# Optimization experiments

Measured on AMD Instinct MI355X. Metric: run time of the kernel, lower is better.

The kernel has to match this reference:

```python
import jax, jax.numpy as jnp
import numpy as np

T, B = 21, 4096
H, E, V = 1024, 50, 96
PAD = 0


def setup_inputs() -> dict:
    key = jax.random.key(0)
    ks = jax.random.split(key, 10)
    s_e = 1.0 / np.sqrt(H)  # torch LSTM init scale
    emb = jax.random.normal(ks[0], (V, E), jnp.float32)
    emb = emb.at[PAD].set(0.0)  # padding_idx row is zero
    return {
        "input_ids": jax.random.randint(ks[1], (T, B), 0, V),
        "h0": jax.random.normal(ks[2], (1, B, H), jnp.float32),
        "c0": jax.random.normal(ks[3], (1, B, H), jnp.float32),
        "emb": emb,
        "W_ih": jax.random.uniform(ks[4], (4 * H, E), jnp.float32, -s_e, s_e),
        "W_hh": jax.random.uniform(ks[5], (4 * H, H), jnp.float32, -s_e, s_e),
        "b_ih": jax.random.uniform(ks[6], (4 * H,), jnp.float32, -s_e, s_e),
        "b_hh": jax.random.uniform(ks[7], (4 * H,), jnp.float32, -s_e, s_e),
        "W_out": jax.random.uniform(ks[8], (V, H), jnp.float32, -s_e, s_e),
        "b_out": jax.random.uniform(ks[9], (V,), jnp.float32, -s_e, s_e),
    }


def reference(input_ids, h0, c0, emb, W_ih, W_hh, b_ih, b_hh, W_out, b_out):
    # char_embeds: (T, B, E)
    x = emb[input_ids]
    # Precompute input projections for all timesteps in one GEMM: (T, B, 4H)
    x_proj = jnp.einsum("tbe,ge->tbg", x, W_ih) + b_ih + b_hh

    def step(carry, xp_t):
        h, c = carry  # (B, H) each
        gates = xp_t + h @ W_hh.T  # (B, 4H), torch gate order i,f,g,o
        i, f, g, o = jnp.split(gates, 4, axis=-1)
        i = jax.nn.sigmoid(i)
        f = jax.nn.sigmoid(f)
        g = jnp.tanh(g)
        o = jax.nn.sigmoid(o)
        c = f * c + i * g
        h = o * jnp.tanh(c)
        return (h, c), h

    (h_T, c_T), h_ts = jax.lax.scan(step, (h0[0], c0[0]), x_proj)
    # char_output_projection: (T, B, V)
    scores = jnp.einsum("tbh,vh->tbv", h_ts, W_out) + b_out
    return scores, (h_T[None], c_T[None])
```

## Files before the change

### kernel.cpp

```cpp
#include <hip/hip_runtime.h>
#include <hip/hip_bf16.h>


#define T_STEPS 21
#define BSZ 4096
#define HDIM 1024
#define VOCAB 96
#define EDIM 50

typedef __attribute__((ext_vector_type(8))) short short8;
typedef __attribute__((ext_vector_type(4))) float f32x4;

#define GLL16(g, l)                                                        \
  __builtin_amdgcn_global_load_lds(                                        \
      (const __attribute__((address_space(1))) void*)(g),                  \
      (__attribute__((address_space(3))) void*)(l), 16, 0, 0)

__device__ __forceinline__ float sigmoidf_fast(float x) {
  return 1.0f / (1.0f + __expf(-x));
}
__device__ __forceinline__ float tanhf_fast(float x) {
  return 2.0f / (1.0f + __expf(-2.0f * x)) - 1.0f;
}

__global__ void prep_convert(const float* __restrict__ Whh_f,
                             const float* __restrict__ Wout_f,
                             const float* __restrict__ h0,
                             __hip_bfloat16* __restrict__ Whh,
                             __hip_bfloat16* __restrict__ Wout,
                             __hip_bfloat16* __restrict__ hb0) {
  int idx = blockIdx.x * 256 + threadIdx.x;
  if (idx < 4 * HDIM * HDIM) {
    Whh[idx] = __float2bfloat16(Whh_f[idx]);
    hb0[idx] = __float2bfloat16(h0[idx]);
  }
  if (idx < VOCAB * HDIM) Wout[idx] = __float2bfloat16(Wout_f[idx]);
}

__global__ void prep_ptable(const float* __restrict__ emb,
                            const float* __restrict__ Wih,
                            const float* __restrict__ bih,
                            const float* __restrict__ bhh,
                            float* __restrict__ P) {
  int idx = blockIdx.x * 256 + threadIdx.x;
  int v = idx >> 12, g = idx & 4095;
  const float* er = emb + v * EDIM;
  const float* wr = Wih + g * EDIM;
  float s = bih[g] + bhh[g];
#pragma unroll 10
  for (int e = 0; e < EDIM; ++e) s += er[e] * wr[e];
  P[idx] = s;
}

template <bool LAST>
__global__ __launch_bounds__(256, 2) void lstm_step_kernel(
    const int* __restrict__ ids,
    const __hip_bfloat16* __restrict__ hprev,
    const __hip_bfloat16* __restrict__ Whh,
    const float* __restrict__ P,
    const float* __restrict__ c_in,
    float* __restrict__ c_out,
    __hip_bfloat16* __restrict__ hnext,
    float* __restrict__ hf32)
{
  __shared__ __align__(16) char smem[49152];
  __hip_bfloat16* sA = (__hip_bfloat16*)smem;
  __hip_bfloat16* sB = (__hip_bfloat16*)(smem + 16384);
  float* sP = (float*)smem;

  const int tid = threadIdx.x;
  const int wave = tid >> 6;
  const int lane = tid & 63;
  const int m0 = blockIdx.x * 128;
  const int j0 = blockIdx.y * 32;

  f32x4 acc[4][4] = {};

  const int lrow = lane >> 3;
  const int lcol = ((lane & 7) ^ lrow) * 8;

  int brow_g[4];
#pragma unroll
  for (int i = 0; i < 4; ++i) {
    int n = wave * 32 + i * 8 + lrow;
    int q = n >> 6, gate = (n >> 4) & 3, u = n & 15;
    brow_g[i] = gate * HDIM + j0 + q * 16 + u;
  }
  const __hip_bfloat16* Abase =
      hprev + (size_t)(m0 + wave * 32 + lrow) * HDIM + lcol;

  const int mw = (wave >> 1) * 64;
  const int nw = (wave & 1) * 64;
  const int u16 = lane & 15;
  const int k16q = lane >> 4;

  for (int k0 = 0; k0 < HDIM; k0 += 64) {
#pragma unroll
    for (int i = 0; i < 4; ++i) {
      GLL16(Abase + i * 8 * HDIM + k0, &sA[(wave * 32 + i * 8) * 64]);
      GLL16(Whh + (size_t)brow_g[i] * HDIM + k0 + lcol,
            &sB[(wave * 32 + i * 8) * 64]);
    }
    __syncthreads();
#pragma unroll
    for (int kk = 0; kk < 64; kk += 32) {
      const int sl = (((kk >> 3) + k16q) ^ (u16 & 7)) * 8;
      short8 af[4], bf[4];
#pragma unroll
      for (int mi = 0; mi < 4; ++mi)
        af[mi] = *(const short8*)&sA[(mw + mi * 16 + u16) * 64 + sl];
#pragma unroll
      for (int ni = 0; ni < 4; ++ni)
        bf[ni] = *(const short8*)&sB[(nw + ni * 16 + u16) * 64 + sl];
#pragma unroll
      for (int mi = 0; mi < 4; ++mi)
#pragma unroll
        for (int ni = 0; ni < 4; ++ni)
          acc[mi][ni] = __builtin_amdgcn_mfma_f32_16x16x32_bf16(
              af[mi], bf[ni], acc[mi][ni], 0, 0, 0);
    }
    __syncthreads();
  }

  {
    const int pchunk = lane & 7;
#pragma unroll
    for (int i = 0; i < 12; ++i) {
      int p = wave * 96 + i * 8 + (lane >> 3);
      int v = p >> 2, gate = p & 3;
      GLL16(P + (size_t)v * 4096 + gate * 1024 + j0 + pchunk * 4,
            &sP[(wave * 96 + i * 8) * 32]);
    }
  }
  __syncthreads();

  const int q = wave & 1;
  const int jo = q * 16 + u16;
  const int j = j0 + jo;
  const int rb = m0 + mw + k16q * 4;
#pragma unroll
  for (int mi = 0; mi < 4; ++mi) {
#pragma unroll
    for (int r = 0; r < 4; ++r) {
      int row = rb + mi * 16 + r;
      int id = ids[row];
      const float* Pr = &sP[id * 128 + jo];
      float iv = acc[mi][0][r] + Pr[0];
      float fv = acc[mi][1][r] + Pr[32];
      float gv = acc[mi][2][r] + Pr[64];
      float ov = acc[mi][3][r] + Pr[96];
      iv = sigmoidf_fast(iv);
      fv = sigmoidf_fast(fv);
      gv = tanhf_fast(gv);
      ov = sigmoidf_fast(ov);
      size_t off = (size_t)row * HDIM + j;
      float cc = fv * c_in[off] + iv * gv;
      c_out[off] = cc;
      float hh = ov * tanhf_fast(cc);
      hnext[off] = __float2bfloat16(hh);
      if (LAST) hf32[off] = hh;
    }
  }
}

__global__ __launch_bounds__(256, 2) void scores_kernel(
    const __hip_bfloat16* __restrict__ h,
    const __hip_bfloat16* __restrict__ Wout,
    const float* __restrict__ bout,
    float* __restrict__ out)
{
  __shared__ __align__(16) __hip_bfloat16 sA[128 * 128];
  __shared__ __align__(16) __hip_bfloat16 sB[96 * 128];

  const int tid = threadIdx.x;
  const int wave = tid >> 6, lane = tid & 63;
  const int u16 = lane & 15, k16q = lane >> 4;
  const long r0 = (long)blockIdx.x * 128;

  f32x4 acc[2][6] = {};

  const int srow4 = lane >> 4;
  const int sslot = lane & 15;

  for (int k0 = 0; k0 < HDIM; k0 += 128) {
#pragma unroll
    for (int i = 0; i < 8; ++i) {
      int row = wave * 32 + i * 4 + srow4;
      int g = sslot ^ (row & 15);
      GLL16(h + (r0 + row) * HDIM + k0 + g * 8, &sA[(wave * 32 + i * 4) * 128]);
    }
#pragma unroll
    for (int i = 0; i < 6; ++i) {
      int row = wave * 24 + i * 4 + srow4;
      int g = sslot ^ (row & 15);
      GLL16(Wout + (size_t)row * HDIM + k0 + g * 8,
            &sB[(wave * 24 + i * 4) * 128]);
    }
    __syncthreads();
#pragma unroll
    for (int kk = 0; kk < 128; kk += 32) {
      const int sl = (((kk >> 3) + k16q) ^ u16) * 8;
      short8 af[2], bf[6];
#pragma unroll
      for (int mi = 0; mi < 2; ++mi)
        af[mi] = *(const short8*)&sA[(wave * 32 + mi * 16 + u16) * 128 + sl];
#pragma unroll
      for (int ni = 0; ni < 6; ++ni)
        bf[ni] = *(const short8*)&sB[(ni * 16 + u16) * 128 + sl];
#pragma unroll
      for (int mi = 0; mi < 2; ++mi)
#pragma unroll
        for (int ni = 0; ni < 6; ++ni)
          acc[mi][ni] = __builtin_amdgcn_mfma_f32_16x16x32_bf16(
              af[mi], bf[ni], acc[mi][ni], 0, 0, 0);
    }
    __syncthreads();
  }

#pragma unroll
  for (int ni = 0; ni < 6; ++ni) {
    int v = ni * 16 + u16;
    float bv = bout[v];
#pragma unroll
    for (int mi = 0; mi < 2; ++mi)
#pragma unroll
      for (int r = 0; r < 4; ++r) {
        long grow = r0 + wave * 32 + mi * 16 + k16q * 4 + r;
        out[grow * VOCAB + v] = acc[mi][ni][r] + bv;
      }
  }
}

extern "C" void kernel_launch(void* const* d_in, const int* in_sizes, int n_in,
                              void* d_out, int out_size, void* d_ws, size_t ws_size,
                              hipStream_t stream) {
  const int* ids = (const int*)d_in[0];
  const float* h0 = (const float*)d_in[1];
  const float* c0 = (const float*)d_in[2];
  const float* emb = (const float*)d_in[3];
  const float* Wih = (const float*)d_in[4];
  const float* Whh_f = (const float*)d_in[5];
  const float* bih = (const float*)d_in[6];
  const float* bhh = (const float*)d_in[7];
  const float* Wout_f = (const float*)d_in[8];
  const float* bout = (const float*)d_in[9];

  float* out = (float*)d_out;
  float* scores = out;
  float* hT = out + (size_t)T_STEPS * BSZ * VOCAB;
  float* cT = hT + (size_t)BSZ * HDIM;

  const size_t BH = (size_t)BSZ * HDIM;
  char* w = (char*)d_ws;
  float* P = (float*)w;              w += (size_t)VOCAB * 4096 * 4;
  __hip_bfloat16* Whh = (__hip_bfloat16*)w;  w += (size_t)4 * HDIM * HDIM * 2;
  __hip_bfloat16* Wout = (__hip_bfloat16*)w; w += (size_t)VOCAB * HDIM * 2;
  __hip_bfloat16* hts = (__hip_bfloat16*)w;
  size_t base = (size_t)VOCAB * 4096 * 4 + (size_t)4 * HDIM * HDIM * 2 +
                (size_t)VOCAB * HDIM * 2;
  const bool full = ws_size >= base + (size_t)(T_STEPS + 1) * BH * 2;

  prep_convert<<<dim3((4 * HDIM * HDIM + 255) / 256), dim3(256), 0, stream>>>(
      Whh_f, Wout_f, h0, Whh, Wout, hts);
  prep_ptable<<<dim3((VOCAB * 4096) / 256), dim3(256), 0, stream>>>(
      emb, Wih, bih, bhh, P);

  for (int t = 0; t < T_STEPS; ++t) {
    __hip_bfloat16* hp = hts + (full ? (size_t)t * BH : (size_t)(t & 1) * BH);
    __hip_bfloat16* hn = hts + (full ? (size_t)(t + 1) * BH : (size_t)((t + 1) & 1) * BH);
    const float* cin = (t == 0) ? c0 : cT;
    if (t == T_STEPS - 1) {
      lstm_step_kernel<true><<<dim3(32, 32), dim3(256), 0, stream>>>(
          ids + (size_t)t * BSZ, hp, Whh, P, cin, cT, hn, hT);
    } else {
      lstm_step_kernel<false><<<dim3(32, 32), dim3(256), 0, stream>>>(
          ids + (size_t)t * BSZ, hp, Whh, P, cin, cT, hn, nullptr);
    }
    if (!full) {
      scores_kernel<<<dim3(BSZ / 128), dim3(256), 0, stream>>>(
          hn, Wout, bout, scores + (size_t)t * BSZ * VOCAB);
    }
  }
  if (full) {
    scores_kernel<<<dim3(T_STEPS * BSZ / 128), dim3(256), 0, stream>>>(
        hts + BH, Wout, bout, scores);
  }
}
```

Measured before the change: 1.208 ms.

## Store input-projection table as bf16 tiled per column block and raise occupancy

```diff
diff --git a/kernel.cpp b/kernel.cpp
--- a/kernel.cpp
+++ b/kernel.cpp
@@ -41,38 +41,43 @@
                             const float* __restrict__ Wih,
                             const float* __restrict__ bih,
                             const float* __restrict__ bhh,
-                            float* __restrict__ P) {
+                            __hip_bfloat16* __restrict__ Pb) {
   int idx = blockIdx.x * 256 + threadIdx.x;
   int v = idx >> 12, g = idx & 4095;
+  int gate = g >> 10, j = g & 1023;
   const float* er = emb + v * EDIM;
   const float* wr = Wih + g * EDIM;
   float s = bih[g] + bhh[g];
 #pragma unroll 10
   for (int e = 0; e < EDIM; ++e) s += er[e] * wr[e];
-  P[idx] = s;
+  Pb[(size_t)(j >> 5) * 12288 + v * 128 + gate * 32 + (j & 31)] =
+      __float2bfloat16(s);
 }
 
 template <bool LAST>
-__global__ __launch_bounds__(256, 2) void lstm_step_kernel(
+__global__ __launch_bounds__(256, 3) void lstm_step_kernel(
     const int* __restrict__ ids,
     const __hip_bfloat16* __restrict__ hprev,
     const __hip_bfloat16* __restrict__ Whh,
-    const float* __restrict__ P,
+    const __hip_bfloat16* __restrict__ Pb,
     const float* __restrict__ c_in,
     float* __restrict__ c_out,
     __hip_bfloat16* __restrict__ hnext,
     float* __restrict__ hf32)
 {
-  __shared__ __align__(16) char smem[49152];
+  __shared__ __align__(16) char smem[32768];
   __hip_bfloat16* sA = (__hip_bfloat16*)smem;
   __hip_bfloat16* sB = (__hip_bfloat16*)(smem + 16384);
-  float* sP = (float*)smem;
+  __hip_bfloat16* sPb = (__hip_bfloat16*)smem;
 
   const int tid = threadIdx.x;
   const int wave = tid >> 6;
   const int lane = tid & 63;
-  const int m0 = blockIdx.x * 128;
-  const int j0 = blockIdx.y * 32;
+  const int bid = blockIdx.x;
+  const int jt = (bid & 7) * 4 + ((bid >> 3) & 3);
+  const int mt = bid >> 5;
+  const int m0 = mt * 128;
+  const int j0 = jt * 32;
 
   f32x4 acc[4][4] = {};
 
@@ -90,9 +95,19 @@
       hprev + (size_t)(m0 + wave * 32 + lrow) * HDIM + lcol;
 
   const int mw = (wave >> 1) * 64;
-  const int nw = (wave & 1) * 64;
+  const int gn = wave & 1;
   const int u16 = lane & 15;
   const int k16q = lane >> 4;
+
+  const int jo = gn * 16 + u16;
+  const int j = j0 + jo;
+  const int rb = m0 + mw + k16q * 4;
+  float cpre[4][4];
+#pragma unroll
+  for (int mi = 0; mi < 4; ++mi)
+#pragma unroll
+    for (int r = 0; r < 4; ++r)
+      cpre[mi][r] = c_in[(size_t)(rb + mi * 16 + r) * HDIM + j];
 
   for (int k0 = 0; k0 < HDIM; k0 += 64) {
 #pragma unroll
@@ -111,7 +126,7 @@
         af[mi] = *(const short8*)&sA[(mw + mi * 16 + u16) * 64 + sl];
 #pragma unroll
       for (int ni = 0; ni < 4; ++ni)
-        bf[ni] = *(const short8*)&sB[(nw + ni * 16 + u16) * 64 + sl];
+        bf[ni] = *(const short8*)&sB[(gn * 64 + ni * 16 + u16) * 64 + sl];
 #pragma unroll
       for (int mi = 0; mi < 4; ++mi)
 #pragma unroll
@@ -123,38 +138,30 @@
   }
 
   {
-    const int pchunk = lane & 7;
-#pragma unroll
-    for (int i = 0; i < 12; ++i) {
-      int p = wave * 96 + i * 8 + (lane >> 3);
-      int v = p >> 2, gate = p & 3;
-      GLL16(P + (size_t)v * 4096 + gate * 1024 + j0 + pchunk * 4,
-            &sP[(wave * 96 + i * 8) * 32]);
-    }
+    const __hip_bfloat16* Pbj = Pb + (size_t)jt * 12288;
+#pragma unroll
+    for (int i = 0; i < 6; ++i)
+      GLL16(Pbj + (wave * 6 + i) * 512 + lane * 8, &sPb[(wave * 6 + i) * 512]);
   }
   __syncthreads();
 
-  const int q = wave & 1;
-  const int jo = q * 16 + u16;
-  const int j = j0 + jo;
-  const int rb = m0 + mw + k16q * 4;
 #pragma unroll
   for (int mi = 0; mi < 4; ++mi) {
 #pragma unroll
     for (int r = 0; r < 4; ++r) {
       int row = rb + mi * 16 + r;
       int id = ids[row];
-      const float* Pr = &sP[id * 128 + jo];
-      float iv = acc[mi][0][r] + Pr[0];
-      float fv = acc[mi][1][r] + Pr[32];
-      float gv = acc[mi][2][r] + Pr[64];
-      float ov = acc[mi][3][r] + Pr[96];
+      const __hip_bfloat16* Pr = &sPb[id * 128 + jo];
+      float iv = acc[mi][0][r] + __bfloat162float(Pr[0]);
+      float fv = acc[mi][1][r] + __bfloat162float(Pr[32]);
+      float gv = acc[mi][2][r] + __bfloat162float(Pr[64]);
+      float ov = acc[mi][3][r] + __bfloat162float(Pr[96]);
       iv = sigmoidf_fast(iv);
       fv = sigmoidf_fast(fv);
       gv = tanhf_fast(gv);
       ov = sigmoidf_fast(ov);
       size_t off = (size_t)row * HDIM + j;
-      float cc = fv * c_in[off] + iv * gv;
+      float cc = fv * cpre[mi][r] + iv * gv;
       c_out[off] = cc;
       float hh = ov * tanhf_fast(cc);
       hnext[off] = __float2bfloat16(hh);
@@ -186,14 +193,14 @@
 #pragma unroll
     for (int i = 0; i < 8; ++i) {
       int row = wave * 32 + i * 4 + srow4;
-      int g = sslot ^ (row & 15);
-      GLL16(h + (r0 + row) * HDIM + k0 + g * 8, &sA[(wave * 32 + i * 4) * 128]);
+      int gg = sslot ^ (row & 15);
+      GLL16(h + (r0 + row) * HDIM + k0 + gg * 8, &sA[(wave * 32 + i * 4) * 128]);
     }
 #pragma unroll
     for (int i = 0; i < 6; ++i) {
       int row = wave * 24 + i * 4 + srow4;
-      int g = sslot ^ (row & 15);
-      GLL16(Wout + (size_t)row * HDIM + k0 + g * 8,
+      int gg = sslot ^ (row & 15);
+      GLL16(Wout + (size_t)row * HDIM + k0 + gg * 8,
             &sB[(wave * 24 + i * 4) * 128]);
     }
     __syncthreads();
@@ -252,29 +259,30 @@
 
   const size_t BH = (size_t)BSZ * HDIM;
   char* w = (char*)d_ws;
-  float* P = (float*)w;              w += (size_t)VOCAB * 4096 * 4;
+  __hip_bfloat16* Pb = (__hip_bfloat16*)w;   w += (size_t)32 * 12288 * 2;
   __hip_bfloat16* Whh = (__hip_bfloat16*)w;  w += (size_t)4 * HDIM * HDIM * 2;
   __hip_bfloat16* Wout = (__hip_bfloat16*)w; w += (size_t)VOCAB * HDIM * 2;
   __hip_bfloat16* hts = (__hip_bfloat16*)w;
-  size_t base = (size_t)VOCAB * 4096 * 4 + (size_t)4 * HDIM * HDIM * 2 +
+  size_t base = (size_t)32 * 12288 * 2 + (size_t)4 * HDIM * HDIM * 2 +
                 (size_t)VOCAB * HDIM * 2;
   const bool full = ws_size >= base + (size_t)(T_STEPS + 1) * BH * 2;
 
   prep_convert<<<dim3((4 * HDIM * HDIM + 255) / 256), dim3(256), 0, stream>>>(
       Whh_f, Wout_f, h0, Whh, Wout, hts);
   prep_ptable<<<dim3((VOCAB * 4096) / 256), dim3(256), 0, stream>>>(
-      emb, Wih, bih, bhh, P);
+      emb, Wih, bih, bhh, Pb);
 
   for (int t = 0; t < T_STEPS; ++t) {
     __hip_bfloat16* hp = hts + (full ? (size_t)t * BH : (size_t)(t & 1) * BH);
-    __hip_bfloat16* hn = hts + (full ? (size_t)(t + 1) * BH : (size_t)((t + 1) & 1) * BH);
+    __hip_bfloat16* hn =
+        hts + (full ? (size_t)(t + 1) * BH : (size_t)((t + 1) & 1) * BH);
     const float* cin = (t == 0) ? c0 : cT;
     if (t == T_STEPS - 1) {
-      lstm_step_kernel<true><<<dim3(32, 32), dim3(256), 0, stream>>>(
-          ids + (size_t)t * BSZ, hp, Whh, P, cin, cT, hn, hT);
+      lstm_step_kernel<true><<<dim3(1024), dim3(256), 0, stream>>>(
+          ids + (size_t)t * BSZ, hp, Whh, Pb, cin, cT, hn, hT);
     } else {
-      lstm_step_kernel<false><<<dim3(32, 32), dim3(256), 0, stream>>>(
-          ids + (size_t)t * BSZ, hp, Whh, P, cin, cT, hn, nullptr);
+      lstm_step_kernel<false><<<dim3(1024), dim3(256), 0, stream>>>(
+          ids + (size_t)t * BSZ, hp, Whh, Pb, cin, cT, hn, nullptr);
     }
     if (!full) {
       scores_kernel<<<dim3(BSZ / 128), dim3(256), 0, stream>>>(
```

Result: no change. 1.188 ms (-1.7%).
